# Performance work log

Hardware: AMD Instinct MI355X
Metric: run time of the kernel (lower is better)

The kernel has to match this reference:

```python
import math
import jax, jax.numpy as jnp
import numpy as np

B, S, D, H = 2, 2048, 768, 12
DK = D // H

def setup_inputs() -> dict:
    key = jax.random.key(0)
    ks = jax.random.split(key, 8)
    scale = 1.0 / math.sqrt(D)
    return {
        "Q": jax.random.normal(ks[0], (B, S, D), dtype=jnp.float32),
        "K": jax.random.normal(ks[1], (B, S, D), dtype=jnp.float32),
        "V": jax.random.normal(ks[2], (B, S, D), dtype=jnp.float32),
        "mask": jax.random.randint(ks[3], (B, 1, S, S), 0, 2, dtype=jnp.int32),
        "W_Q": jax.random.normal(ks[4], (D, D), dtype=jnp.float32) * scale,
        "W_K": jax.random.normal(ks[5], (D, D), dtype=jnp.float32) * scale,
        "W_V": jax.random.normal(ks[6], (D, D), dtype=jnp.float32) * scale,
        "W_O": jax.random.normal(ks[7], (D, D), dtype=jnp.float32) * scale,
    }

def reference(Q, K, V, mask, W_Q, W_K, W_V, W_O):
    # torch Linear: y = x @ W.T (weight shape [out, in], no bias)
    q = (Q @ W_Q.T).reshape(B, S, H, DK).transpose(0, 2, 1, 3)  # [B,H,S,dk]
    k = (K @ W_K.T).reshape(B, S, H, DK).transpose(0, 2, 1, 3)
    v = (V @ W_V.T).reshape(B, S, H, DK).transpose(0, 2, 1, 3)
    scores = jnp.einsum('bhqd,bhkd->bhqk', q, k) / math.sqrt(DK)
    scores = jnp.where(mask == 0, -jnp.inf, scores)
    weights = jax.nn.softmax(scores, axis=-1)
    weights = jnp.nan_to_num(weights, nan=0.0)
    out = jnp.einsum('bhqk,bhkd->bhqd', weights, v)  # [B,H,S,dk]
    out = out.transpose(0, 2, 1, 3).reshape(B, S, D)
    return out @ W_O.T
```

## Files before the change

### kernel.cpp

```cpp
#include <hip/hip_runtime.h>
#include <hip/hip_bf16.h>
#include <stdint.h>

typedef __attribute__((ext_vector_type(8))) short bf16x8;
typedef __attribute__((ext_vector_type(4))) short bf16x4;
typedef __attribute__((ext_vector_type(4))) float f32x4;
typedef __attribute__((ext_vector_type(16))) float f32x16;
typedef __attribute__((ext_vector_type(4))) unsigned short u16x4;

__device__ __forceinline__ unsigned short f2bf(float x) {
  union { __hip_bfloat16 h; unsigned short s; } u;
  u.h = __float2bfloat16(x);
  return u.s;
}
__device__ __forceinline__ unsigned int cvtpk(float lo, float hi) {
  unsigned int r;
  asm("v_cvt_pk_bf16_f32 %0, %1, %2" : "=v"(r) : "v"(lo), "v"(hi));
  return r;
}
__device__ __forceinline__ void gll16(const unsigned short* g, unsigned short* l) {
  __builtin_amdgcn_global_load_lds(
      (const __attribute__((address_space(1))) unsigned int*)g,
      (__attribute__((address_space(3))) unsigned int*)l, 16, 0, 0);
}

__global__ __launch_bounds__(256) void maskpack_kernel(const int* __restrict__ mask,
                                                       unsigned int* __restrict__ mp,
                                                       int total) {
  int i = blockIdx.x * blockDim.x + threadIdx.x;
  const int lane = threadIdx.x & 63;
  const int stride = gridDim.x * blockDim.x;
  for (; i < total; i += stride) {
    unsigned long long b = __ballot(mask[i] != 0);
    if (lane == 0)       mp[i >> 5] = (unsigned int)b;
    else if (lane == 32) mp[i >> 5] = (unsigned int)(b >> 32);
  }
}

__global__ __launch_bounds__(256) void precast_kernel(
    const float* __restrict__ q, const float* __restrict__ k, const float* __restrict__ v,
    const float* __restrict__ wq, const float* __restrict__ wk, const float* __restrict__ wv,
    const float* __restrict__ wo,
    unsigned short* __restrict__ qb, unsigned short* __restrict__ kb, unsigned short* __restrict__ vb,
    unsigned short* __restrict__ wqb, unsigned short* __restrict__ wkb,
    unsigned short* __restrict__ wvb, unsigned short* __restrict__ wob) {
  const int U = 1474560;
  for (int u = blockIdx.x * blockDim.x + threadIdx.x; u < U; u += gridDim.x * blockDim.x) {
    const float* s; unsigned short* d; int r; float scale = 1.0f;
    if (u < 1179648) {
      int which = u / 393216; r = u - which * 393216;
      s = (which == 0) ? q : (which == 1) ? k : v;
      d = (which == 0) ? qb : (which == 1) ? kb : vb;
    } else {
      int u2 = u - 1179648; int which = u2 / 73728; r = u2 - which * 73728;
      s = (which == 0) ? wq : (which == 1) ? wk : (which == 2) ? wv : wo;
      d = (which == 0) ? wqb : (which == 1) ? wkb : (which == 2) ? wvb : wob;
      if (which == 0) scale = 0.18033688f;
    }
    float4 a = *(const float4*)&s[(size_t)r * 8];
    float4 b2 = *(const float4*)&s[(size_t)r * 8 + 4];
    uint4 o;
    o.x = cvtpk(a.x * scale, a.y * scale);
    o.y = cvtpk(a.z * scale, a.w * scale);
    o.z = cvtpk(b2.x * scale, b2.y * scale);
    o.w = cvtpk(b2.z * scale, b2.w * scale);
    *(uint4*)&d[(size_t)r * 8] = o;
  }
}

#define GEMM_BODY(AEXPR, BEXPR)                                                   \
  __shared__ unsigned short As[2][128][32];                                       \
  __shared__ unsigned short Bs[2][128][32];                                       \
  const int m0 = blockIdx.y * 128, n0 = blockIdx.x * 128;                         \
  const int t = threadIdx.x, lane = t & 63, w = t >> 6;                           \
  const int wr = w >> 1, wc = w & 1, fr = lane & 15, cl = lane >> 4;              \
  const int srl = lane >> 2, sph = lane & 3;                                      \
  f32x4 acc[4][4] = {};                                                           \
  auto ISSUE = [&](int kk, int buf) {                                             \
    _Pragma("unroll")                                                             \
    for (int i = 0; i < 2; ++i) {                                                 \
      const int row = i * 64 + w * 16 + srl;                                      \
      const int c = sph ^ ((row >> 1) & 3);                                       \
      gll16(AEXPR, &As[buf][i * 64 + w * 16][0]);                                 \
      gll16(BEXPR, &Bs[buf][i * 64 + w * 16][0]);                                 \
    }                                                                             \
  };                                                                              \
  ISSUE(0, 0);                                                                    \
  asm volatile("s_waitcnt vmcnt(0)" ::: "memory");                                \
  __syncthreads();                                                                \
  for (int it = 0; it < 24; ++it) {                                               \
    const int buf = it & 1;                                                       \
    if (it < 23) ISSUE((it + 1) * 32, buf ^ 1);                                   \
    bf16x8 af[4], bfr[4];                                                         \
    _Pragma("unroll")                                                             \
    for (int i = 0; i < 4; ++i) {                                                 \
      const int R = wr * 64 + i * 16 + fr;                                        \
      af[i] = *(const bf16x8*)&As[buf][R][(cl ^ ((R >> 1) & 3)) * 8];             \
    }                                                                             \
    _Pragma("unroll")                                                             \
    for (int j = 0; j < 4; ++j) {                                                 \
      const int R = wc * 64 + j * 16 + fr;                                        \
      bfr[j] = *(const bf16x8*)&Bs[buf][R][(cl ^ ((R >> 1) & 3)) * 8];            \
    }                                                                             \
    __builtin_amdgcn_s_setprio(1);                                                \
    _Pragma("unroll")                                                             \
    for (int i = 0; i < 4; ++i)                                                   \
      _Pragma("unroll")                                                           \
      for (int j = 0; j < 4; ++j)                                                 \
        acc[i][j] = __builtin_amdgcn_mfma_f32_16x16x32_bf16(af[i], bfr[j],        \
                                                            acc[i][j], 0, 0, 0); \
    __builtin_amdgcn_s_setprio(0);                                                \
    asm volatile("s_waitcnt vmcnt(0)" ::: "memory");                              \
    __syncthreads();                                                              \
  }

__global__ __launch_bounds__(256) void proj_b16(
    const unsigned short* __restrict__ Qb, const unsigned short* __restrict__ Kb,
    const unsigned short* __restrict__ Vb,
    const unsigned short* __restrict__ Wqb, const unsigned short* __restrict__ Wkb,
    const unsigned short* __restrict__ Wvb,
    unsigned short* __restrict__ qo, unsigned short* __restrict__ ko,
    unsigned short* __restrict__ vo) {
  const int z = blockIdx.z;
  const unsigned short* A = (z == 0) ? Qb : (z == 1) ? Kb : Vb;
  const unsigned short* W = (z == 0) ? Wqb : (z == 1) ? Wkb : Wvb;
  GEMM_BODY(A + (size_t)(m0 + row) * 768 + kk + c * 8,
            W + (size_t)(n0 + row) * 768 + kk + c * 8)
  if (z == 2) {
    for (int i = 0; i < 4; ++i)
      for (int j = 0; j < 4; ++j) {
        int m = m0 + wr * 64 + i * 16 + (lane >> 4) * 4;
        int n = n0 + wc * 64 + j * 16 + fr;
        int b = m >> 11, s = m & 2047, hd = n >> 6, dk = n & 63;
        u16x4 pk;
        for (int r = 0; r < 4; ++r) pk[r] = f2bf(acc[i][j][r]);
        *(u16x4*)&vo[((size_t)(b * 12 + hd) * 64 + dk) * 2048 + s] = pk;
      }
  } else {
    unsigned short* O = (z == 0) ? qo : ko;
    for (int i = 0; i < 4; ++i)
      for (int j = 0; j < 4; ++j)
        for (int r = 0; r < 4; ++r) {
          int m = m0 + wr * 64 + i * 16 + (lane >> 4) * 4 + r;
          int n = n0 + wc * 64 + j * 16 + fr;
          int b = m >> 11, s = m & 2047, hd = n >> 6, dk = n & 63;
          O[((size_t)(b * 12 + hd) * 2048 + s) * 64 + dk] = f2bf(acc[i][j][r]);
        }
  }
}

__global__ __launch_bounds__(256) void out_b16(
    const unsigned short* __restrict__ Ain, const unsigned short* __restrict__ Wob,
    float* __restrict__ Out) {
  GEMM_BODY(Ain + (size_t)(m0 + row) * 768 + kk + c * 8,
            Wob + (size_t)(n0 + row) * 768 + kk + c * 8)
  for (int i = 0; i < 4; ++i)
    for (int j = 0; j < 4; ++j)
      for (int r = 0; r < 4; ++r) {
        int m = m0 + wr * 64 + i * 16 + (lane >> 4) * 4 + r;
        int n = n0 + wc * 64 + j * 16 + fr;
        Out[(size_t)m * 768 + n] = acc[i][j][r];
      }
}

__global__ __launch_bounds__(256) void proj_gemm(
    const float* __restrict__ Qi, const float* __restrict__ Ki, const float* __restrict__ Vi,
    const float* __restrict__ Wq, const float* __restrict__ Wk, const float* __restrict__ Wv,
    unsigned short* __restrict__ qo, unsigned short* __restrict__ ko, unsigned short* __restrict__ vo) {
  constexpr int LDT = 56;
  __shared__ unsigned short As[128][LDT];
  __shared__ unsigned short Bs[128][LDT];
  const int z = blockIdx.z;
  const float* A = (z == 0) ? Qi : (z == 1) ? Ki : Vi;
  const float* W = (z == 0) ? Wq : (z == 1) ? Wk : Wv;
  const int m0 = blockIdx.y * 128, n0 = blockIdx.x * 128;
  const int t = threadIdx.x, lane = t & 63, w = t >> 6;
  const int wr = w >> 1, wc = w & 1;
  const int fr = lane & 15, fg = (lane >> 4) * 8;
  const int srow = t >> 3, sseg = t & 7;
  f32x4 acc[4][4] = {};
  for (int kk = 0; kk < 768; kk += 32) {
    for (int pp = 0; pp < 4; ++pp) {
      int row = srow + pp * 32;
      float4 fa = *(const float4*)&A[(size_t)(m0 + row) * 768 + kk + sseg * 4];
      float4 fb = *(const float4*)&W[(size_t)(n0 + row) * 768 + kk + sseg * 4];
      bf16x4 pa = {(short)f2bf(fa.x), (short)f2bf(fa.y), (short)f2bf(fa.z), (short)f2bf(fa.w)};
      bf16x4 pb = {(short)f2bf(fb.x), (short)f2bf(fb.y), (short)f2bf(fb.z), (short)f2bf(fb.w)};
      *(bf16x4*)&As[row][sseg * 4] = pa;
      *(bf16x4*)&Bs[row][sseg * 4] = pb;
    }
    __syncthreads();
    bf16x8 af[4], bfr[4];
    for (int i = 0; i < 4; ++i) af[i]  = *(const bf16x8*)&As[wr * 64 + i * 16 + fr][fg];
    for (int i = 0; i < 4; ++i) bfr[i] = *(const bf16x8*)&Bs[wc * 64 + i * 16 + fr][fg];
    for (int i = 0; i < 4; ++i)
      for (int j = 0; j < 4; ++j)
        acc[i][j] = __builtin_amdgcn_mfma_f32_16x16x32_bf16(af[i], bfr[j], acc[i][j], 0, 0, 0);
    __syncthreads();
  }
  if (z == 2) {
    for (int i = 0; i < 4; ++i)
      for (int j = 0; j < 4; ++j) {
        int m = m0 + wr * 64 + i * 16 + (lane >> 4) * 4;
        int n = n0 + wc * 64 + j * 16 + fr;
        int b = m >> 11, s = m & 2047, hd = n >> 6, dk = n & 63;
        u16x4 pk;
        for (int r = 0; r < 4; ++r) pk[r] = f2bf(acc[i][j][r]);
        *(u16x4*)&vo[((size_t)(b * 12 + hd) * 64 + dk) * 2048 + s] = pk;
      }
  } else {
    unsigned short* O = (z == 0) ? qo : ko;
    const float scale = (z == 0) ? 0.18033688f : 1.0f;
    for (int i = 0; i < 4; ++i)
      for (int j = 0; j < 4; ++j)
        for (int r = 0; r < 4; ++r) {
          int m = m0 + wr * 64 + i * 16 + (lane >> 4) * 4 + r;
          int n = n0 + wc * 64 + j * 16 + fr;
          int b = m >> 11, s = m & 2047, hd = n >> 6, dk = n & 63;
          O[((size_t)(b * 12 + hd) * 2048 + s) * 64 + dk] = f2bf(acc[i][j][r] * scale);
        }
  }
}

__global__ __launch_bounds__(256) void out_gemm(
    const unsigned short* __restrict__ Ain, const float* __restrict__ W,
    float* __restrict__ Out) {
  constexpr int LDT = 56;
  __shared__ unsigned short As[128][LDT];
  __shared__ unsigned short Bs[128][LDT];
  const int m0 = blockIdx.y * 128, n0 = blockIdx.x * 128;
  const int t = threadIdx.x, lane = t & 63, w = t >> 6;
  const int wr = w >> 1, wc = w & 1;
  const int fr = lane & 15, fg = (lane >> 4) * 8;
  f32x4 acc[4][4] = {};
  for (int kk = 0; kk < 768; kk += 32) {
    {
      int row = t >> 2, seg = t & 3;
      for (int pp = 0; pp < 2; ++pp) {
        bf16x8 va = *(const bf16x8*)&Ain[(size_t)(m0 + row + pp * 64) * 768 + kk + seg * 8];
        *(bf16x8*)&As[row + pp * 64][seg * 8] = va;
      }
      int row2 = t >> 3, seg2 = t & 7;
      for (int pp = 0; pp < 4; ++pp) {
        float4 fb = *(const float4*)&W[(size_t)(n0 + row2 + pp * 32) * 768 + kk + seg2 * 4];
        bf16x4 pb = {(short)f2bf(fb.x), (short)f2bf(fb.y), (short)f2bf(fb.z), (short)f2bf(fb.w)};
        *(bf16x4*)&Bs[row2 + pp * 32][seg2 * 4] = pb;
      }
    }
    __syncthreads();
    bf16x8 af[4], bfr[4];
    for (int i = 0; i < 4; ++i) af[i]  = *(const bf16x8*)&As[wr * 64 + i * 16 + fr][fg];
    for (int i = 0; i < 4; ++i) bfr[i] = *(const bf16x8*)&Bs[wc * 64 + i * 16 + fr][fg];
    for (int i = 0; i < 4; ++i)
      for (int j = 0; j < 4; ++j)
        acc[i][j] = __builtin_amdgcn_mfma_f32_16x16x32_bf16(af[i], bfr[j], acc[i][j], 0, 0, 0);
    __syncthreads();
  }
  for (int i = 0; i < 4; ++i)
    for (int j = 0; j < 4; ++j)
      for (int r = 0; r < 4; ++r) {
        int m = m0 + wr * 64 + i * 16 + (lane >> 4) * 4 + r;
        int n = n0 + wc * 64 + j * 16 + fr;
        Out[(size_t)m * 768 + n] = acc[i][j][r];
      }
}

__global__ __launch_bounds__(512) void attn_kernel(
    const unsigned short* __restrict__ qh, const unsigned short* __restrict__ kh,
    const unsigned short* __restrict__ vh, const unsigned int* __restrict__ mp,
    unsigned short* __restrict__ ao) {
  __shared__ union LdsU {
    struct {
      unsigned short K[2][4][32][64];
      unsigned short V[2][4][64][32];
    } st;
    float M[8][32][64];
  } lds;
  __shared__ float Sm[8][64];
  __shared__ float Sl[8][64];
  const int t = threadIdx.x, lane = t & 63, w = t >> 6;
  const int wq = w & 1, sp = w >> 1;
  const int bid = blockIdx.x;
  const int xcd = bid & 7, idx = bid >> 3;
  const int bh = xcd * 3 + (idx >> 5);
  const int qb = idx & 31;
  const int bb = bh / 12, hh = bh % 12;
  const int qc = lane & 31, h = lane >> 5;
  const int q = qb * 64 + wq * 32 + qc;
  const unsigned short* qrow = qh + ((size_t)bh * 2048 + q) * 64;
  bf16x8 bq[4];
#pragma unroll
  for (int kc = 0; kc < 4; ++kc) bq[kc] = *(const bf16x8*)(qrow + kc * 16 + h * 8);
  const unsigned int* mrow = mp + ((size_t)bb * 2048 + q) * 64 + sp * 16;
  const unsigned short* kgb = kh + (size_t)bh * 2048 * 64;
  const unsigned short* vgb = vh + (size_t)bh * 64 * 2048;
  f32x16 acc0 = {}, acc1 = {};
  float l_run = 0.f;
  float m_run = -1e30f;
  const int KT0 = sp * 512;
  const int krow = lane >> 3, ksch = (lane & 7) ^ (lane >> 3);
  const int vrow = lane >> 2, vsch = (lane & 3) ^ ((lane >> 3) & 3);
  auto ISSUE = [&](int it2, int b2) {
    const int KT = KT0 + it2 * 32;
    unsigned short* kd = &lds.st.K[b2][sp][0][0];
    unsigned short* vd = &lds.st.V[b2][sp][0][0];
#pragma unroll
    for (int c2 = 0; c2 < 2; ++c2) {
      const int c = 2 * wq + c2;
      gll16(kgb + (size_t)(KT + c * 8 + krow) * 64 + ksch * 8, kd + c * 512);
    }
#pragma unroll
    for (int c2 = 0; c2 < 2; ++c2) {
      const int c = 2 * wq + c2;
      gll16(vgb + (size_t)(c * 16 + vrow) * 2048 + KT + vsch * 8, vd + c * 512);
    }
  };
  ISSUE(0, 0);
#pragma unroll 2
  for (int it = 0; it < 16; ++it) {
    const int b = it & 1;
    asm volatile("s_waitcnt vmcnt(0)" ::: "memory");
    __syncthreads();
    if (it < 15) ISSUE(it + 1, b ^ 1);
    const unsigned int m32 = mrow[it];
    bf16x8 ka[4];
#pragma unroll
    for (int kc = 0; kc < 4; ++kc)
      ka[kc] = *(const bf16x8*)&lds.st.K[b][sp][qc][((kc * 2 + h) ^ (qc & 7)) * 8];
    f32x16 sc = {};
    __builtin_amdgcn_s_setprio(1);
#pragma unroll
    for (int kc = 0; kc < 4; ++kc)
      sc = __builtin_amdgcn_mfma_f32_32x32x16_bf16(ka[kc], bq[kc], sc, 0, 0, 0);
    __builtin_amdgcn_s_setprio(0);
    bf16x8 va0[2], va1[2];
#pragma unroll
    for (int ks = 0; ks < 2; ++ks) {
      const int cs = ((ks * 2 + h) ^ ((qc >> 1) & 3)) * 8;
      va0[ks] = *(const bf16x8*)&lds.st.V[b][sp][qc][cs];
      va1[ks] = *(const bf16x8*)&lds.st.V[b][sp][32 + qc][cs];
    }
    const unsigned int wsh = m32 >> (4 * h);
#pragma unroll
    for (int r = 0; r < 16; ++r) {
      const int sh = (r & 3) + 8 * (r >> 2);
      sc[r] = ((wsh >> sh) & 1u) ? sc[r] : -3.0e38f;
    }
    float mA0 = fmaxf(fmaxf(sc[0], sc[4]), fmaxf(sc[8], sc[12]));
    float mA1 = fmaxf(fmaxf(sc[1], sc[5]), fmaxf(sc[9], sc[13]));
    float mA2 = fmaxf(fmaxf(sc[2], sc[6]), fmaxf(sc[10], sc[14]));
    float mA3 = fmaxf(fmaxf(sc[3], sc[7]), fmaxf(sc[11], sc[15]));
    float m1 = fmaxf(fmaxf(mA0, mA1), fmaxf(mA2, mA3));
    float tmax = fmaxf(m1, __shfl_xor(m1, 32, 64));
    if (__any(tmax > m_run + 8.0f)) {
      float mnew = fmaxf(m_run, tmax);
      float scl = exp2f(m_run - mnew);
      m_run = mnew;
      l_run *= scl;
#pragma unroll
      for (int e = 0; e < 16; ++e) { acc0[e] *= scl; acc1[e] *= scl; }
    }
#pragma unroll
    for (int r = 0; r < 16; ++r) sc[r] = exp2f(sc[r] - m_run);
    float sA0 = (sc[0] + sc[4]) + (sc[8] + sc[12]);
    float sA1 = (sc[1] + sc[5]) + (sc[9] + sc[13]);
    float sA2 = (sc[2] + sc[6]) + (sc[10] + sc[14]);
    float sA3 = (sc[3] + sc[7]) + (sc[11] + sc[15]);
    float s1 = (sA0 + sA1) + (sA2 + sA3);
    l_run += s1 + __shfl_xor(s1, 32, 64);
    __builtin_amdgcn_s_setprio(1);
#define PVQ(P, OFF, A0, A1) { \
    unsigned int a0 = cvtpk(P[OFF + 0], P[OFF + 1]), a1 = cvtpk(P[OFF + 2], P[OFF + 3]); \
    unsigned int b0 = cvtpk(P[OFF + 4], P[OFF + 5]), b1 = cvtpk(P[OFF + 6], P[OFF + 7]); \
    asm("v_permlane32_swap_b32 %0, %1" : "+v"(a0), "+v"(b0)); \
    asm("v_permlane32_swap_b32 %0, %1" : "+v"(a1), "+v"(b1)); \
    union { unsigned int u[4]; bf16x8 v; } bfu; \
    bfu.u[0] = a0; bfu.u[1] = a1; bfu.u[2] = b0; bfu.u[3] = b1; \
    acc0 = __builtin_amdgcn_mfma_f32_32x32x16_bf16(A0, bfu.v, acc0, 0, 0, 0); \
    acc1 = __builtin_amdgcn_mfma_f32_32x32x16_bf16(A1, bfu.v, acc1, 0, 0, 0); }
    PVQ(sc, 0, va0[0], va1[0]);
    PVQ(sc, 8, va0[1], va1[1]);
#undef PVQ
    __builtin_amdgcn_s_setprio(0);
  }
  __syncthreads();
  Sm[w][lane] = m_run;
  Sl[w][lane] = l_run;
#pragma unroll
  for (int e = 0; e < 16; ++e) lds.M[w][e][lane] = acc0[e];
#pragma unroll
  for (int e = 0; e < 16; ++e) lds.M[w][16 + e][lane] = acc1[e];
  __syncthreads();
  float pm0 = Sm[wq][lane],     pm1 = Sm[2 + wq][lane];
  float pm2 = Sm[4 + wq][lane], pm3 = Sm[6 + wq][lane];
  float M = fmaxf(fmaxf(pm0, pm1), fmaxf(pm2, pm3));
  float w0 = exp2f(pm0 - M), w1 = exp2f(pm1 - M), w2 = exp2f(pm2 - M), w3 = exp2f(pm3 - M);
  float L = Sl[wq][lane] * w0 + Sl[2 + wq][lane] * w1 +
            Sl[4 + wq][lane] * w2 + Sl[6 + wq][lane] * w3;
  float inv = (L > 0.f) ? 1.0f / L : 0.f;
  unsigned short* orow = ao + ((size_t)bb * 2048 + q) * 768 + hh * 64;
#pragma unroll
  for (int g = 0; g < 2; ++g) {
    const int e0 = sp * 8 + g * 4;
    const int base = (e0 >= 16) ? 32 : 0;
    const int er0 = e0 & 15;
    const int d0 = base + 8 * (er0 >> 2) + 4 * h;
    u16x4 pk4;
#pragma unroll
    for (int j = 0; j < 4; ++j) {
      float v = (lds.M[wq][e0 + j][lane] * w0 + lds.M[2 + wq][e0 + j][lane] * w1 +
                 lds.M[4 + wq][e0 + j][lane] * w2 + lds.M[6 + wq][e0 + j][lane] * w3) * inv;
      pk4[j] = f2bf(v);
    }
    *(u16x4*)&orow[d0] = pk4;
  }
}

extern "C" void kernel_launch(void* const* d_in, const int* in_sizes, int n_in,
                              void* d_out, int out_size, void* d_ws, size_t ws_size,
                              hipStream_t stream) {
  const float* Q  = (const float*)d_in[0];
  const float* K  = (const float*)d_in[1];
  const float* V  = (const float*)d_in[2];
  const int*   mask = (const int*)d_in[3];
  const float* WQ = (const float*)d_in[4];
  const float* WK = (const float*)d_in[5];
  const float* WV = (const float*)d_in[6];
  const float* WO = (const float*)d_in[7];
  float* out = (float*)d_out;
  char* ws = (char*)d_ws;

  const size_t NEED = 43515904ull;
  if (ws_size >= NEED) {
    unsigned short* qh  = (unsigned short*)(ws + 0);
    unsigned short* kh  = (unsigned short*)(ws + 6291456);
    unsigned short* vh  = (unsigned short*)(ws + 12582912);
    unsigned int*   mp  = (unsigned int*)(ws + 18874368);
    unsigned short* Qb  = (unsigned short*)(ws + 19922944);
    unsigned short* ao  = Qb;
    unsigned short* Kb  = (unsigned short*)(ws + 26214400);
    unsigned short* Vb  = (unsigned short*)(ws + 32505856);
    unsigned short* Wqb = (unsigned short*)(ws + 38797312);
    unsigned short* Wkb = (unsigned short*)(ws + 39976960);
    unsigned short* Wvb = (unsigned short*)(ws + 41156608);
    unsigned short* Wob = (unsigned short*)(ws + 42336256);
    maskpack_kernel<<<dim3(2048), 256, 0, stream>>>(mask, mp, 2 * 2048 * 2048);
    precast_kernel<<<dim3(2880), 256, 0, stream>>>(Q, K, V, WQ, WK, WV, WO,
                                                   Qb, Kb, Vb, Wqb, Wkb, Wvb, Wob);
    proj_b16<<<dim3(6, 32, 3), 256, 0, stream>>>(Qb, Kb, Vb, Wqb, Wkb, Wvb, qh, kh, vh);
    attn_kernel<<<dim3(768), 512, 0, stream>>>(qh, kh, vh, mp, ao);
    out_b16<<<dim3(6, 32), 256, 0, stream>>>(ao, Wob, out);
  } else {
    unsigned short* qh = (unsigned short*)(ws + 0);
    unsigned short* kh = (unsigned short*)(ws + 6291456);
    unsigned short* vh = (unsigned short*)(ws + 12582912);
    unsigned short* ao = (unsigned short*)(ws + 18874368);
    unsigned int*   mp = (unsigned int*)(ws + 25165824);
    maskpack_kernel<<<dim3(2048), 256, 0, stream>>>(mask, mp, 2 * 2048 * 2048);
    proj_gemm<<<dim3(6, 32, 3), 256, 0, stream>>>(Q, K, V, WQ, WK, WV, qh, kh, vh);
    attn_kernel<<<dim3(768), 512, 0, stream>>>(qh, kh, vh, mp, ao);
    out_gemm<<<dim3(6, 32), 256, 0, stream>>>(ao, WO, out);
  }
}
```

Measured before the change: 149.9 us.

## Merge mask-pack and precast kernels, single-buffer V and halve attention LDS

Fuses the mask bit-packing and bf16 precast into one launch so the two independent prep jobs share one grid and drop one kernel launch. In the attention kernel, V is now single-buffered and loaded after the PV step of each iteration behind an extra barrier. The final cross-wave reduction is done in two halves through a 16-row scratch buffer. Together these shrink shared memory per block, presumably to allow more resident blocks, at the cost of an extra sync per iteration and less overlap of the V load.

New measurement: 185.2 us. +23.6%, slower.

```diff
diff --git a/kernel.cpp b/kernel.cpp
--- a/kernel.cpp
+++ b/kernel.cpp
@@ -22,6 +22,50 @@
   __builtin_amdgcn_global_load_lds(
       (const __attribute__((address_space(1))) unsigned int*)g,
       (__attribute__((address_space(3))) unsigned int*)l, 16, 0, 0);
+}
+
+__global__ __launch_bounds__(256) void prep_kernel(
+    const int* __restrict__ mask, unsigned int* __restrict__ mp,
+    const float* __restrict__ q, const float* __restrict__ k, const float* __restrict__ v,
+    const float* __restrict__ wq, const float* __restrict__ wk, const float* __restrict__ wv,
+    const float* __restrict__ wo,
+    unsigned short* __restrict__ qb, unsigned short* __restrict__ kb, unsigned short* __restrict__ vb,
+    unsigned short* __restrict__ wqb, unsigned short* __restrict__ wkb,
+    unsigned short* __restrict__ wvb, unsigned short* __restrict__ wob) {
+  if (blockIdx.x < 2048) {
+    const int total = 2 * 2048 * 2048;
+    const int lane = threadIdx.x & 63;
+    const int stride = 2048 * 256;
+    for (int i = blockIdx.x * 256 + threadIdx.x; i < total; i += stride) {
+      unsigned long long b = __ballot(mask[i] != 0);
+      if (lane == 0)       mp[i >> 5] = (unsigned int)b;
+      else if (lane == 32) mp[i >> 5] = (unsigned int)(b >> 32);
+    }
+  } else {
+    const int U = 1474560;
+    const int stride = 2880 * 256;
+    for (int u = (blockIdx.x - 2048) * 256 + threadIdx.x; u < U; u += stride) {
+      const float* s; unsigned short* d; int r; float scale = 1.0f;
+      if (u < 1179648) {
+        int which = u / 393216; r = u - which * 393216;
+        s = (which == 0) ? q : (which == 1) ? k : v;
+        d = (which == 0) ? qb : (which == 1) ? kb : vb;
+      } else {
+        int u2 = u - 1179648; int which = u2 / 73728; r = u2 - which * 73728;
+        s = (which == 0) ? wq : (which == 1) ? wk : (which == 2) ? wv : wo;
+        d = (which == 0) ? wqb : (which == 1) ? wkb : (which == 2) ? wvb : wob;
+        if (which == 0) scale = 0.18033688f;
+      }
+      float4 a = *(const float4*)&s[(size_t)r * 8];
+      float4 b2 = *(const float4*)&s[(size_t)r * 8 + 4];
+      uint4 o;
+      o.x = cvtpk(a.x * scale, a.y * scale);
+      o.y = cvtpk(a.z * scale, a.w * scale);
+      o.z = cvtpk(b2.x * scale, b2.y * scale);
+      o.w = cvtpk(b2.z * scale, b2.w * scale);
+      *(uint4*)&d[(size_t)r * 8] = o;
+    }
+  }
 }
 
 __global__ __launch_bounds__(256) void maskpack_kernel(const int* __restrict__ mask,
@@ -34,37 +78,6 @@
     unsigned long long b = __ballot(mask[i] != 0);
     if (lane == 0)       mp[i >> 5] = (unsigned int)b;
     else if (lane == 32) mp[i >> 5] = (unsigned int)(b >> 32);
-  }
-}
-
-__global__ __launch_bounds__(256) void precast_kernel(
-    const float* __restrict__ q, const float* __restrict__ k, const float* __restrict__ v,
-    const float* __restrict__ wq, const float* __restrict__ wk, const float* __restrict__ wv,
-    const float* __restrict__ wo,
-    unsigned short* __restrict__ qb, unsigned short* __restrict__ kb, unsigned short* __restrict__ vb,
-    unsigned short* __restrict__ wqb, unsigned short* __restrict__ wkb,
-    unsigned short* __restrict__ wvb, unsigned short* __restrict__ wob) {
-  const int U = 1474560;
-  for (int u = blockIdx.x * blockDim.x + threadIdx.x; u < U; u += gridDim.x * blockDim.x) {
-    const float* s; unsigned short* d; int r; float scale = 1.0f;
-    if (u < 1179648) {
-      int which = u / 393216; r = u - which * 393216;
-      s = (which == 0) ? q : (which == 1) ? k : v;
-      d = (which == 0) ? qb : (which == 1) ? kb : vb;
-    } else {
-      int u2 = u - 1179648; int which = u2 / 73728; r = u2 - which * 73728;
-      s = (which == 0) ? wq : (which == 1) ? wk : (which == 2) ? wv : wo;
-      d = (which == 0) ? wqb : (which == 1) ? wkb : (which == 2) ? wvb : wob;
-      if (which == 0) scale = 0.18033688f;
-    }
-    float4 a = *(const float4*)&s[(size_t)r * 8];
-    float4 b2 = *(const float4*)&s[(size_t)r * 8 + 4];
-    uint4 o;
-    o.x = cvtpk(a.x * scale, a.y * scale);
-    o.y = cvtpk(a.z * scale, a.w * scale);
-    o.z = cvtpk(b2.x * scale, b2.y * scale);
-    o.w = cvtpk(b2.z * scale, b2.w * scale);
-    *(uint4*)&d[(size_t)r * 8] = o;
   }
 }
 
@@ -272,9 +285,9 @@
   __shared__ union LdsU {
     struct {
       unsigned short K[2][4][32][64];
-      unsigned short V[2][4][64][32];
+      unsigned short V[4][64][32];
     } st;
-    float M[8][32][64];
+    float M16[8][16][64];
   } lds;
   __shared__ float Sm[8][64];
   __shared__ float Sl[8][64];
@@ -300,28 +313,32 @@
   const int KT0 = sp * 512;
   const int krow = lane >> 3, ksch = (lane & 7) ^ (lane >> 3);
   const int vrow = lane >> 2, vsch = (lane & 3) ^ ((lane >> 3) & 3);
-  auto ISSUE = [&](int it2, int b2) {
+  auto ISSUE_K = [&](int it2, int b2) {
     const int KT = KT0 + it2 * 32;
     unsigned short* kd = &lds.st.K[b2][sp][0][0];
-    unsigned short* vd = &lds.st.V[b2][sp][0][0];
 #pragma unroll
     for (int c2 = 0; c2 < 2; ++c2) {
       const int c = 2 * wq + c2;
       gll16(kgb + (size_t)(KT + c * 8 + krow) * 64 + ksch * 8, kd + c * 512);
     }
+  };
+  auto ISSUE_V = [&](int it2) {
+    const int KT = KT0 + it2 * 32;
+    unsigned short* vd = &lds.st.V[sp][0][0];
 #pragma unroll
     for (int c2 = 0; c2 < 2; ++c2) {
       const int c = 2 * wq + c2;
       gll16(vgb + (size_t)(c * 16 + vrow) * 2048 + KT + vsch * 8, vd + c * 512);
     }
   };
-  ISSUE(0, 0);
+  ISSUE_K(0, 0);
+  ISSUE_V(0);
 #pragma unroll 2
   for (int it = 0; it < 16; ++it) {
     const int b = it & 1;
     asm volatile("s_waitcnt vmcnt(0)" ::: "memory");
     __syncthreads();
-    if (it < 15) ISSUE(it + 1, b ^ 1);
+    if (it < 15) ISSUE_K(it + 1, b ^ 1);
     const unsigned int m32 = mrow[it];
     bf16x8 ka[4];
 #pragma unroll
@@ -337,8 +354,8 @@
 #pragma unroll
     for (int ks = 0; ks < 2; ++ks) {
       const int cs = ((ks * 2 + h) ^ ((qc >> 1) & 3)) * 8;
-      va0[ks] = *(const bf16x8*)&lds.st.V[b][sp][qc][cs];
-      va1[ks] = *(const bf16x8*)&lds.st.V[b][sp][32 + qc][cs];
+      va0[ks] = *(const bf16x8*)&lds.st.V[sp][qc][cs];
+      va1[ks] = *(const bf16x8*)&lds.st.V[sp][32 + qc][cs];
     }
     const unsigned int wsh = m32 >> (4 * h);
 #pragma unroll
@@ -382,14 +399,13 @@
     PVQ(sc, 8, va0[1], va1[1]);
 #undef PVQ
     __builtin_amdgcn_s_setprio(0);
-  }
-  __syncthreads();
+    __syncthreads();
+    if (it < 15) ISSUE_V(it + 1);
+  }
   Sm[w][lane] = m_run;
   Sl[w][lane] = l_run;
 #pragma unroll
-  for (int e = 0; e < 16; ++e) lds.M[w][e][lane] = acc0[e];
-#pragma unroll
-  for (int e = 0; e < 16; ++e) lds.M[w][16 + e][lane] = acc1[e];
+  for (int e = 0; e < 16; ++e) lds.M16[w][e][lane] = acc0[e];
   __syncthreads();
   float pm0 = Sm[wq][lane],     pm1 = Sm[2 + wq][lane];
   float pm2 = Sm[4 + wq][lane], pm3 = Sm[6 + wq][lane];
@@ -399,20 +415,41 @@
             Sl[4 + wq][lane] * w2 + Sl[6 + wq][lane] * w3;
   float inv = (L > 0.f) ? 1.0f / L : 0.f;
   unsigned short* orow = ao + ((size_t)bb * 2048 + q) * 768 + hh * 64;
-#pragma unroll
-  for (int g = 0; g < 2; ++g) {
-    const int e0 = sp * 8 + g * 4;
-    const int base = (e0 >= 16) ? 32 : 0;
-    const int er0 = e0 & 15;
-    const int d0 = base + 8 * (er0 >> 2) + 4 * h;
-    u16x4 pk4;
-#pragma unroll
-    for (int j = 0; j < 4; ++j) {
-      float v = (lds.M[wq][e0 + j][lane] * w0 + lds.M[2 + wq][e0 + j][lane] * w1 +
-                 lds.M[4 + wq][e0 + j][lane] * w2 + lds.M[6 + wq][e0 + j][lane] * w3) * inv;
-      pk4[j] = f2bf(v);
-    }
-    *(u16x4*)&orow[d0] = pk4;
+  if (sp < 2) {
+    const int e0 = sp * 8;
+#pragma unroll
+    for (int g = 0; g < 2; ++g) {
+      u16x4 pk4;
+#pragma unroll
+      for (int j = 0; j < 4; ++j) {
+        const int e = e0 + g * 4 + j;
+        float v = (lds.M16[wq][e][lane] * w0 + lds.M16[2 + wq][e][lane] * w1 +
+                   lds.M16[4 + wq][e][lane] * w2 + lds.M16[6 + wq][e][lane] * w3) * inv;
+        pk4[j] = f2bf(v);
+      }
+      const int d0 = 8 * ((e0 + g * 4) >> 2) + 4 * h;
+      *(u16x4*)&orow[d0] = pk4;
+    }
+  }
+  __syncthreads();
+#pragma unroll
+  for (int e = 0; e < 16; ++e) lds.M16[w][e][lane] = acc1[e];
+  __syncthreads();
+  if (sp >= 2) {
+    const int e0 = (sp - 2) * 8;
+#pragma unroll
+    for (int g = 0; g < 2; ++g) {
+      u16x4 pk4;
+#pragma unroll
+      for (int j = 0; j < 4; ++j) {
+        const int e = e0 + g * 4 + j;
+        float v = (lds.M16[wq][e][lane] * w0 + lds.M16[2 + wq][e][lane] * w1 +
+                   lds.M16[4 + wq][e][lane] * w2 + lds.M16[6 + wq][e][lane] * w3) * inv;
+        pk4[j] = f2bf(v);
+      }
+      const int d0 = 32 + 8 * ((e0 + g * 4) >> 2) + 4 * h;
+      *(u16x4*)&orow[d0] = pk4;
+    }
   }
 }
 
@@ -444,9 +481,8 @@
     unsigned short* Wkb = (unsigned short*)(ws + 39976960);
     unsigned short* Wvb = (unsigned short*)(ws + 41156608);
     unsigned short* Wob = (unsigned short*)(ws + 42336256);
-    maskpack_kernel<<<dim3(2048), 256, 0, stream>>>(mask, mp, 2 * 2048 * 2048);
-    precast_kernel<<<dim3(2880), 256, 0, stream>>>(Q, K, V, WQ, WK, WV, WO,
-                                                   Qb, Kb, Vb, Wqb, Wkb, Wvb, Wob);
+    prep_kernel<<<dim3(4928), 256, 0, stream>>>(mask, mp, Q, K, V, WQ, WK, WV, WO,
+                                                Qb, Kb, Vb, Wqb, Wkb, Wvb, Wob);
     proj_b16<<<dim3(6, 32, 3), 256, 0, stream>>>(Qb, Kb, Vb, Wqb, Wkb, Wvb, qh, kh, vh);
     attn_kernel<<<dim3(768), 512, 0, stream>>>(qh, kh, vh, mp, ao);
     out_b16<<<dim3(6, 32), 256, 0, stream>>>(ao, Wob, out);
```
